# Performance work log

Measured on AMD Instinct MI355X. Metric: run time of the kernel, lower is better.

The kernel has to match this reference:

```python
import jax, jax.numpy as jnp
import numpy as np

N_NODES = 100000
IN_F = 256
OUT_F = 256
BATCH = 50000
NUM_SAMPLES = 25


def setup_inputs() -> dict:
    key = jax.random.key(0)
    k1, k2, k3, k4 = jax.random.split(key, 4)
    features = jax.random.normal(k1, (N_NODES, IN_F), dtype=jnp.float32)
    node_idx = jax.random.randint(k2, (BATCH,), 0, N_NODES, dtype=jnp.int64 if jax.config.jax_enable_x64 else jnp.int32)
    neigh_idx = jax.random.randint(k3, (BATCH, NUM_SAMPLES), 0, N_NODES, dtype=jnp.int64 if jax.config.jax_enable_x64 else jnp.int32)
    # Linear(2*in_features, out_features, bias=False); torch stores weight as [out, 2*in],
    # we store W as [out, 2*in] transposed to [2*in, out] for x @ W.
    init_range = np.sqrt(6.0 / (2 * IN_F + OUT_F))
    W = jax.random.uniform(k4, (OUT_F, 2 * IN_F), dtype=jnp.float32, minval=-init_range, maxval=init_range)
    return {"features": features, "node_idx": node_idx, "neigh_idx": neigh_idx, "W": W}


def reference(features, node_idx, neigh_idx, W):
    # self features: [B, in]
    self_feat = features[node_idx]
    # gather + mean over sampled neighbors: [B, S, in] -> [B, in]
    neigh_mean = jnp.mean(features[neigh_idx], axis=1)
    # concat and project: [B, 2*in] @ [2*in, out]
    combined = jnp.concatenate([self_feat, neigh_mean], axis=1)
    return combined @ W.T
```

## Files before the change

### kernel.cpp

```cpp
#include <hip/hip_runtime.h>

#define N_NODES 100000
#define IN_F    256
#define OUT_F   256
#define BATCH   50000
#define NSAMP   25
#define K2      512
#define NTILE_N 1563
#define NTILE_B 782
#define XS      256

typedef _Float16 f16_t;
typedef f16_t f16x8 __attribute__((ext_vector_type(8)));
typedef float f32x4 __attribute__((ext_vector_type(4)));
typedef float f32x2 __attribute__((ext_vector_type(2)));
typedef __bf16 bf16_t;
typedef bf16_t bf16x8 __attribute__((ext_vector_type(8)));

#if defined(__has_builtin)
#if __has_builtin(__builtin_amdgcn_cvt_pk_f32_fp8) && __has_builtin(__builtin_amdgcn_cvt_pk_fp8_f32)
#define FP8_HW 1
#endif
#endif
#ifndef FP8_HW
#include <hip/hip_fp8.h>
#endif

#define P8_OFF   25600000L
#define WG_OFF   51200000L
#define WS_NEED  (WG_OFF + 512L * 256 * 2)

__device__ __forceinline__ float h2f(unsigned short u) {
    union { unsigned short u; f16_t h; } t; t.u = u; return (float)t.h;
}

__device__ __forceinline__ unsigned int pk_fp8x4(float a, float b, float c, float d) {
#ifdef FP8_HW
    unsigned int r = __builtin_amdgcn_cvt_pk_fp8_f32(a, b, 0u, false);
    r = __builtin_amdgcn_cvt_pk_fp8_f32(c, d, r, true);
    return r;
#else
    union { unsigned char b[4]; unsigned int u; } t;
    t.b[0] = __hip_fp8_e4m3(a).__x; t.b[1] = __hip_fp8_e4m3(b).__x;
    t.b[2] = __hip_fp8_e4m3(c).__x; t.b[3] = __hip_fp8_e4m3(d).__x;
    return t.u;
#endif
}

__device__ __forceinline__ void acc_fp8x4(unsigned int v, float4& a) {
#ifdef FP8_HW
    f32x2 lo = __builtin_amdgcn_cvt_pk_f32_fp8(v, false);
    f32x2 hi = __builtin_amdgcn_cvt_pk_f32_fp8(v, true);
    a.x += lo[0]; a.y += lo[1]; a.z += hi[0]; a.w += hi[1];
#else
    union { unsigned int u; unsigned char b[4]; } t; t.u = v;
    __hip_fp8_e4m3 e0, e1, e2, e3;
    e0.__x = t.b[0]; e1.__x = t.b[1]; e2.__x = t.b[2]; e3.__x = t.b[3];
    a.x += (float)e0; a.y += (float)e1; a.z += (float)e2; a.w += (float)e3;
#endif
}

__global__ void wconv(const float* __restrict__ W, f16_t* __restrict__ Wg) {
    int idx = blockIdx.x * 256 + threadIdx.x;
    int j = idx >> 8, k = idx & 255;
    float v = (j < 256) ? W[j * K2 + k] : W[(j - 256) * K2 + 256 + k];
    Wg[idx] = (f16_t)v;
}

__global__ __launch_bounds__(512, 2) void proj_gemm(
    const float* __restrict__ features, const f16_t* __restrict__ Wg,
    const int* __restrict__ node_idx,
    f16_t* __restrict__ Pselfb, unsigned char* __restrict__ Pneigh8)
{
    __shared__ unsigned short buf[2][64 * 256];
    const int tid = threadIdx.x, lane = tid & 63, w = tid >> 6;
    const int q16 = lane >> 4, r16 = lane & 15;
    const int ycg = blockIdx.y;
    const int c0 = (ycg == 0 ? 256 : 0) + w * 32;
    const int ntile = (ycg == 0) ? NTILE_N : NTILE_B;
    const int rmax  = (ycg == 0) ? N_NODES : BATCH;
    const int row_s = tid >> 3;
    const int seg_s = tid & 7;

    f16x8 wgall[8][2];
    #pragma unroll
    for (int s = 0; s < 8; ++s)
        #pragma unroll
        for (int ct = 0; ct < 2; ++ct)
            wgall[s][ct] = *(const f16x8*)&Wg[(long)(c0 + ct * 16 + r16) * 256 + s * 32 + q16 * 8];

    f32x4 acc[2][4];
    #pragma unroll
    for (int ct = 0; ct < 2; ++ct)
        #pragma unroll
        for (int rt = 0; rt < 4; ++rt) acc[ct][rt] = (f32x4){0.f, 0.f, 0.f, 0.f};

    float4 v[8];

#define VLOAD(TT)                                                               \
    {                                                                           \
        long rr_ = (long)(TT) * 64 + row_s;                                     \
        if (rr_ > rmax - 1) rr_ = rmax - 1;                                     \
        const long sr_ = (ycg == 0) ? rr_ : (long)node_idx[rr_];                \
        const float* p_ = &features[sr_ * IN_F + seg_s * 32];                   \
        _Pragma("unroll")                                                       \
        for (int j_ = 0; j_ < 8; ++j_) v[j_] = *(const float4*)(p_ + j_ * 4);   \
    }

    VLOAD(blockIdx.x);
    int cur = 0;

    for (int t = blockIdx.x; t < ntile; t += XS) {
        #pragma unroll
        for (int p = 0; p < 4; ++p) {
            const int g  = seg_s * 4 + p;
            const int gp = g ^ (row_s & 7);
            f16x8 hh;
            hh[0] = (f16_t)v[2 * p].x;     hh[1] = (f16_t)v[2 * p].y;
            hh[2] = (f16_t)v[2 * p].z;     hh[3] = (f16_t)v[2 * p].w;
            hh[4] = (f16_t)v[2 * p + 1].x; hh[5] = (f16_t)v[2 * p + 1].y;
            hh[6] = (f16_t)v[2 * p + 1].z; hh[7] = (f16_t)v[2 * p + 1].w;
            *(f16x8*)&buf[cur][row_s * 256 + gp * 8] = hh;
        }
        __syncthreads();

        if (t + XS < ntile) VLOAD(t + XS);

        #pragma unroll
        for (int sg = 0; sg < 8; ++sg) {
            f16x8 bfr[4];
            #pragma unroll
            for (int rt = 0; rt < 4; ++rt) {
                const int row = rt * 16 + r16;
                const int g   = (sg * 4 + q16) ^ (row & 7);
                bfr[rt] = *(const f16x8*)&buf[cur][row * 256 + g * 8];
            }
            #pragma unroll
            for (int ct = 0; ct < 2; ++ct)
                #pragma unroll
                for (int rt = 0; rt < 4; ++rt)
                    acc[ct][rt] = __builtin_amdgcn_mfma_f32_16x16x32_f16(
                        wgall[sg][ct], bfr[rt], acc[ct][rt], 0, 0, 0);
        }

        const long gr0 = (long)t * 64;
        if (ycg == 0) {
            #pragma unroll
            for (int rt = 0; rt < 4; ++rt) {
                const long row = gr0 + rt * 16 + r16;
                const bool ok = row < N_NODES;
                #pragma unroll
                for (int ct = 0; ct < 2; ++ct) {
                    const int colb = w * 32 + ct * 16 + q16 * 4;
                    unsigned int pk = pk_fp8x4(acc[ct][rt][0], acc[ct][rt][1],
                                               acc[ct][rt][2], acc[ct][rt][3]);
                    if (ok) *(unsigned int*)&Pneigh8[row * 256 + colb] = pk;
                }
            }
        } else {
            #pragma unroll
            for (int rt = 0; rt < 4; ++rt) {
                const long b = gr0 + rt * 16 + r16;
                const bool ok = b < BATCH;
                #pragma unroll
                for (int ct = 0; ct < 2; ++ct) {
                    const int colb = w * 32 + ct * 16 + q16 * 4;
                    if (ok) {
                        union { ushort4 u; f16_t hh[4]; } tt;
                        tt.hh[0] = (f16_t)acc[ct][rt][0]; tt.hh[1] = (f16_t)acc[ct][rt][1];
                        tt.hh[2] = (f16_t)acc[ct][rt][2]; tt.hh[3] = (f16_t)acc[ct][rt][3];
                        *(ushort4*)&Pselfb[b * 256 + colb] = tt.u;
                    }
                }
            }
        }
        #pragma unroll
        for (int ct = 0; ct < 2; ++ct)
            #pragma unroll
            for (int rt = 0; rt < 4; ++rt) acc[ct][rt] = (f32x4){0.f, 0.f, 0.f, 0.f};
        cur ^= 1;
    }
#undef VLOAD
}

__global__ __launch_bounds__(256) void gather_add(
    const f16_t* __restrict__ Pselfb, const unsigned char* __restrict__ P8,
    const int* __restrict__ neigh_idx, float* __restrict__ out)
{
    const int tid = threadIdx.x, lane = tid & 63, w = tid >> 6;
    const long b0 = (long)blockIdx.x * 8 + w * 2;
    const int c4 = lane * 4;

    int ns0[NSAMP], ns1[NSAMP];
    #pragma unroll
    for (int s = 0; s < NSAMP; ++s) ns0[s] = neigh_idx[b0 * NSAMP + s];
    #pragma unroll
    for (int s = 0; s < NSAMP; ++s) ns1[s] = neigh_idx[(b0 + 1) * NSAMP + s];

    const ushort4 sv0 = *(const ushort4*)&Pselfb[b0 * 256 + c4];
    const ushort4 sv1 = *(const ushort4*)&Pselfb[(b0 + 1) * 256 + c4];

    unsigned int v0[NSAMP], v1[NSAMP];
    #pragma unroll
    for (int s = 0; s < NSAMP; ++s)
        v0[s] = *(const unsigned int*)&P8[(long)ns0[s] * 256 + c4];
    #pragma unroll
    for (int s = 0; s < NSAMP; ++s)
        v1[s] = *(const unsigned int*)&P8[(long)ns1[s] * 256 + c4];

    float4 a0 = make_float4(0.f, 0.f, 0.f, 0.f);
    float4 a1 = make_float4(0.f, 0.f, 0.f, 0.f);
    #pragma unroll
    for (int s = 0; s < NSAMP; ++s) acc_fp8x4(v0[s], a0);
    #pragma unroll
    for (int s = 0; s < NSAMP; ++s) acc_fp8x4(v1[s], a1);

    const float inv = 1.0f / (float)NSAMP;
    float4 o0, o1;
    o0.x = h2f(sv0.x) + a0.x * inv; o0.y = h2f(sv0.y) + a0.y * inv;
    o0.z = h2f(sv0.z) + a0.z * inv; o0.w = h2f(sv0.w) + a0.w * inv;
    o1.x = h2f(sv1.x) + a1.x * inv; o1.y = h2f(sv1.y) + a1.y * inv;
    o1.z = h2f(sv1.z) + a1.z * inv; o1.w = h2f(sv1.w) + a1.w * inv;
    *(float4*)&out[b0 * OUT_F + c4] = o0;
    *(float4*)&out[(b0 + 1) * OUT_F + c4] = o1;
}

__device__ __forceinline__ int swz_bf(int row, int us_idx) {
    return us_idx ^ ((row & 7) << 3);
}
__device__ __forceinline__ void store_bf4(unsigned short* comb, int r, int col, float4 f) {
    union { ushort4 u; bf16_t b[4]; } t;
    t.b[0] = (bf16_t)f.x; t.b[1] = (bf16_t)f.y;
    t.b[2] = (bf16_t)f.z; t.b[3] = (bf16_t)f.w;
    *(ushort4*)&comb[swz_bf(r, r * K2 + col)] = t.u;
}
__global__ __launch_bounds__(256, 4) void sage_fused(
    const float* __restrict__ features, const int* __restrict__ node_idx,
    const int* __restrict__ neigh_idx, const float* __restrict__ W,
    float* __restrict__ out)
{
    __shared__ unsigned short comb[16 * K2];
    const int tid = threadIdx.x, lane = tid & 63, wy = tid >> 6;
    const int b0 = blockIdx.x * 16;
    const int col4 = lane * 4;
    #pragma unroll
    for (int i = 0; i < 4; ++i) {
        const int r = wy * 4 + i;
        const long b = b0 + r;
        int nidx[NSAMP];
        #pragma unroll
        for (int s = 0; s < NSAMP; ++s) nidx[s] = neigh_idx[b * NSAMP + s];
        const int self_n = node_idx[b];
        const float4 sf = *(const float4*)&features[(long)self_n * IN_F + col4];
        float4 v[13];
        #pragma unroll
        for (int s = 0; s < 13; ++s)
            v[s] = *(const float4*)&features[(long)nidx[s] * IN_F + col4];
        float4 acc = v[0];
        #pragma unroll
        for (int s = 1; s < 13; ++s) {
            acc.x += v[s].x; acc.y += v[s].y; acc.z += v[s].z; acc.w += v[s].w;
        }
        #pragma unroll
        for (int s = 13; s < NSAMP; ++s)
            v[s - 13] = *(const float4*)&features[(long)nidx[s] * IN_F + col4];
        #pragma unroll
        for (int s = 0; s < 12; ++s) {
            acc.x += v[s].x; acc.y += v[s].y; acc.z += v[s].z; acc.w += v[s].w;
        }
        const float inv = 1.0f / (float)NSAMP;
        acc.x *= inv; acc.y *= inv; acc.z *= inv; acc.w *= inv;
        store_bf4(comb, r, col4, sf);
        store_bf4(comb, r, IN_F + col4, acc);
    }
    __syncthreads();
    const int c0 = wy * 64, arow = lane & 15, kq = (lane >> 4) * 8;
    f32x4 acc[4];
    #pragma unroll
    for (int t = 0; t < 4; ++t) acc[t] = (f32x4){0.f, 0.f, 0.f, 0.f};
    #pragma unroll
    for (int ks = 0; ks < 16; ++ks) {
        const int kb = ks * 32 + kq;
        const bf16x8 af = *(const bf16x8*)&comb[swz_bf(arow, arow * K2 + kb)];
        #pragma unroll
        for (int t = 0; t < 4; ++t) {
            const float* wp = &W[(long)(c0 + t * 16 + arow) * K2 + kb];
            const float4 w0 = *(const float4*)wp;
            const float4 w1 = *(const float4*)(wp + 4);
            bf16x8 bf;
            bf[0] = (bf16_t)w0.x; bf[1] = (bf16_t)w0.y;
            bf[2] = (bf16_t)w0.z; bf[3] = (bf16_t)w0.w;
            bf[4] = (bf16_t)w1.x; bf[5] = (bf16_t)w1.y;
            bf[6] = (bf16_t)w1.z; bf[7] = (bf16_t)w1.w;
            acc[t] = __builtin_amdgcn_mfma_f32_16x16x32_bf16(af, bf, acc[t], 0, 0, 0);
        }
    }
    #pragma unroll
    for (int t = 0; t < 4; ++t) {
        const int col = c0 + t * 16 + arow;
        #pragma unroll
        for (int j = 0; j < 4; ++j) {
            const int row = b0 + (lane >> 4) * 4 + j;
            out[(long)row * OUT_F + col] = acc[t][j];
        }
    }
}

extern "C" void kernel_launch(void* const* d_in, const int* in_sizes, int n_in,
                              void* d_out, int out_size, void* d_ws, size_t ws_size,
                              hipStream_t stream) {
    const float* features  = (const float*)d_in[0];
    const int*   node_idx  = (const int*)d_in[1];
    const int*   neigh_idx = (const int*)d_in[2];
    const float* W         = (const float*)d_in[3];
    float*       out       = (float*)d_out;

    if (ws_size >= (size_t)WS_NEED) {
        f16_t*         Pselfb = (f16_t*)d_ws;
        unsigned char* P8     = (unsigned char*)d_ws + P8_OFF;
        f16_t*         Wg     = (f16_t*)((char*)d_ws + WG_OFF);
        wconv<<<512, 256, 0, stream>>>(W, Wg);
        proj_gemm<<<dim3(XS, 2), 512, 0, stream>>>(features, Wg, node_idx, Pselfb, P8);
        gather_add<<<BATCH / 8, 256, 0, stream>>>(Pselfb, P8, neigh_idx, out);
    } else {
        sage_fused<<<BATCH / 16, 256, 0, stream>>>(features, node_idx, neigh_idx, W, out);
    }
}
```

Baseline: 114.4 us.

## Balance projection GEMM tiles across a single flattened block grid

Replaces the 2D grid where one half of the blocks processed all node tiles and the other half the batch self tiles with a 1D grid striding over a concatenated tile range. Blocks reload their weight fragment from global memory when they cross from node tiles to batch tiles. This aims to remove the imbalance where node-tile blocks did nearly twice the work of self-tile blocks, at the cost of occasional weight register reloads and extra per-tile branching.

```diff
diff --git a/kernel.cpp b/kernel.cpp
--- a/kernel.cpp
+++ b/kernel.cpp
@@ -8,7 +8,8 @@
 #define K2      512
 #define NTILE_N 1563
 #define NTILE_B 782
-#define XS      256
+#define NTILE_T (NTILE_N + NTILE_B)
+#define NBLK    512
 
 typedef _Float16 f16_t;
 typedef f16_t f16x8 __attribute__((ext_vector_type(8)));
@@ -75,19 +76,20 @@
     __shared__ unsigned short buf[2][64 * 256];
     const int tid = threadIdx.x, lane = tid & 63, w = tid >> 6;
     const int q16 = lane >> 4, r16 = lane & 15;
-    const int ycg = blockIdx.y;
-    const int c0 = (ycg == 0 ? 256 : 0) + w * 32;
-    const int ntile = (ycg == 0) ? NTILE_N : NTILE_B;
-    const int rmax  = (ycg == 0) ? N_NODES : BATCH;
     const int row_s = tid >> 3;
     const int seg_s = tid & 7;
 
     f16x8 wgall[8][2];
-    #pragma unroll
-    for (int s = 0; s < 8; ++s)
-        #pragma unroll
-        for (int ct = 0; ct < 2; ++ct)
-            wgall[s][ct] = *(const f16x8*)&Wg[(long)(c0 + ct * 16 + r16) * 256 + s * 32 + q16 * 8];
+#define LOADWG(H)                                                               \
+    {                                                                           \
+        const int c0_ = ((H) ? 0 : 256) + w * 32;                               \
+        _Pragma("unroll")                                                       \
+        for (int s_ = 0; s_ < 8; ++s_)                                          \
+            _Pragma("unroll")                                                   \
+            for (int ct_ = 0; ct_ < 2; ++ct_)                                   \
+                wgall[s_][ct_] = *(const f16x8*)                                \
+                    &Wg[(long)(c0_ + ct_ * 16 + r16) * 256 + s_ * 32 + q16 * 8]; \
+    }
 
     f32x4 acc[2][4];
     #pragma unroll
@@ -99,18 +101,29 @@
 
 #define VLOAD(TT)                                                               \
     {                                                                           \
-        long rr_ = (long)(TT) * 64 + row_s;                                     \
-        if (rr_ > rmax - 1) rr_ = rmax - 1;                                     \
-        const long sr_ = (ycg == 0) ? rr_ : (long)node_idx[rr_];                \
+        long sr_;                                                               \
+        if ((TT) >= NTILE_N) {                                                  \
+            long b_ = (long)((TT) - NTILE_N) * 64 + row_s;                      \
+            if (b_ > BATCH - 1) b_ = BATCH - 1;                                 \
+            sr_ = (long)node_idx[b_];                                           \
+        } else {                                                                \
+            sr_ = (long)(TT) * 64 + row_s;                                      \
+            if (sr_ > N_NODES - 1) sr_ = N_NODES - 1;                           \
+        }                                                                       \
         const float* p_ = &features[sr_ * IN_F + seg_s * 32];                   \
         _Pragma("unroll")                                                       \
         for (int j_ = 0; j_ < 8; ++j_) v[j_] = *(const float4*)(p_ + j_ * 4);   \
     }
 
+    int curhalf = (blockIdx.x >= NTILE_N) ? 1 : 0;
+    LOADWG(curhalf);
     VLOAD(blockIdx.x);
     int cur = 0;
 
-    for (int t = blockIdx.x; t < ntile; t += XS) {
+    for (int t = blockIdx.x; t < NTILE_T; t += NBLK) {
+        const int th = (t >= NTILE_N) ? 1 : 0;
+        if (th != curhalf) { curhalf = th; LOADWG(th); }
+
         #pragma unroll
         for (int p = 0; p < 4; ++p) {
             const int g  = seg_s * 4 + p;
@@ -124,7 +137,7 @@
         }
         __syncthreads();
 
-        if (t + XS < ntile) VLOAD(t + XS);
+        if (t + NBLK < NTILE_T) VLOAD(t + NBLK);
 
         #pragma unroll
         for (int sg = 0; sg < 8; ++sg) {
@@ -143,8 +156,8 @@
                         wgall[sg][ct], bfr[rt], acc[ct][rt], 0, 0, 0);
         }
 
-        const long gr0 = (long)t * 64;
-        if (ycg == 0) {
+        if (th == 0) {
+            const long gr0 = (long)t * 64;
             #pragma unroll
             for (int rt = 0; rt < 4; ++rt) {
                 const long row = gr0 + rt * 16 + r16;
@@ -158,6 +171,7 @@
                 }
             }
         } else {
+            const long gr0 = (long)(t - NTILE_N) * 64;
             #pragma unroll
             for (int rt = 0; rt < 4; ++rt) {
                 const long b = gr0 + rt * 16 + r16;
@@ -181,6 +195,7 @@
         cur ^= 1;
     }
 #undef VLOAD
+#undef LOADWG
 }
 
 __global__ __launch_bounds__(256) void gather_add(
@@ -320,7 +335,7 @@
         unsigned char* P8     = (unsigned char*)d_ws + P8_OFF;
         f16_t*         Wg     = (f16_t*)((char*)d_ws + WG_OFF);
         wconv<<<512, 256, 0, stream>>>(W, Wg);
-        proj_gemm<<<dim3(XS, 2), 512, 0, stream>>>(features, Wg, node_idx, Pselfb, P8);
+        proj_gemm<<<NBLK, 512, 0, stream>>>(features, Wg, node_idx, Pselfb, P8);
         gather_add<<<BATCH / 8, 256, 0, stream>>>(Pselfb, P8, neigh_idx, out);
     } else {
         sage_fused<<<BATCH / 16, 256, 0, stream>>>(features, node_idx, neigh_idx, W, out);
```

Result: slower. 121.9 us (+6.6%).
